# Optimization experiments

Measured on AMD Instinct MI355X. Metric: run time of the kernel, lower is better.

The kernel has to match this reference:

```python
import jax, jax.numpy as jnp
import numpy as np
from jax import lax

NB, NS, C, H, W = 16, 8, 3, 128, 128
FVDIM, K = 512, 10


def setup_inputs() -> dict:
    key = jax.random.key(0)
    ks = jax.random.split(key, 5)
    x = jax.random.normal(ks[0], (NB, NS, C, H, W), dtype=jnp.float32)
    nslice = jax.random.randint(ks[1], (NB,), 1, NS + 1, dtype=jnp.int64)  # at least 1 valid slice
    conv_w = jax.random.normal(ks[2], (FVDIM, C, 7, 7), dtype=jnp.float32) * 0.05
    conv_b = jnp.zeros((FVDIM,), dtype=jnp.float32)
    q0 = jnp.ones((1, FVDIM), dtype=jnp.float32)  # L1Aggregator init: ones
    proj_w = jax.random.normal(ks[3], (K, FVDIM), dtype=jnp.float32) * 0.02
    proj_b = jnp.zeros((K,), dtype=jnp.float32)
    return {"x": x, "nslice": nslice, "conv_w": conv_w, "conv_b": conv_b,
            "q0": q0, "proj_w": proj_w, "proj_b": proj_b}


def _extract(x, conv_w, conv_b):
    # stand-in for extractor.Resnet(4): conv(7x7, stride 4) -> ReLU -> global avg pool
    nb, ns = x.shape[:2]
    xf = x.reshape(nb * ns, C, H, W)
    y = lax.conv_general_dilated(xf, conv_w, (4, 4), 'SAME',
                                 dimension_numbers=('NCHW', 'OIHW', 'NCHW'))
    y = jax.nn.relu(y + conv_b[None, :, None, None])
    fvs = jnp.mean(y, axis=(2, 3))          # (nb*ns, fvdim)
    return fvs.reshape(nb, ns, FVDIM)


def reference(x, nslice, conv_w, conv_b, q0, proj_w, proj_b):
    # x: (nb, ns, c, h, w); ragged over ns via nslice -> masked batched attention
    fvs = _extract(x, conv_w, conv_b)                       # (nb, ns, d)
    mask = jnp.arange(NS)[None, :] < nslice[:, None]        # (nb, ns)
    scores = jnp.einsum('d,bsd->bs', q0[0], fvs)            # ek = q0 @ fvs^T per sample
    scores = jnp.where(mask, scores, -jnp.inf)
    ak = jax.nn.softmax(scores, axis=1)                     # per-sample softmax over valid slices
    r0 = jnp.einsum('bs,bsd->bd', ak, fvs)                  # (nb, d)
    return jax.nn.sigmoid(r0 @ proj_w.T + proj_b)           # (nb, k)
```

## Files before the change

### kernel.cpp

```cpp
#include <hip/hip_runtime.h>

#define NB 16
#define NS 8
#define NIMG (NB*NS)
#define CIN 3
#define HWDIM 128
#define FV 512
#define KOUT 10
#define STRIPS 4
#define WIN_ROWS (CIN*35)
#define WIN_STRIDE 136
#define NKT 6
#define WTB_ELEMS (NKT*32*64*8)

typedef __attribute__((ext_vector_type(8))) short bf16x8;
typedef __attribute__((ext_vector_type(4))) float f32x4;

__device__ __forceinline__ unsigned short f2bf(float f) {
    unsigned int u = __float_as_uint(f);
    u = (u + 0x7FFFu + ((u >> 16) & 1u)) >> 16;
    return (unsigned short)u;
}

__global__ void wprep_kernel(const float* __restrict__ cw,
                             unsigned short* __restrict__ wtb) {
    int i = blockIdx.x * 256 + threadIdx.x;
    int j  = i & 7;
    int l  = (i >> 3) & 63;
    int nt = (i >> 9) & 31;
    int kt = i >> 14;
    int oc = nt * 16 + (l & 15);
    int kb = kt * 4 + (l >> 4);
    unsigned short v = 0;
    if (kb < 21 && j < 7) {
        int ic = kb / 7, ky = kb - 7 * ic;
        v = f2bf(cw[(size_t)oc * 147 + ic * 49 + ky * 7 + j]);
    }
    wtb[i] = v;
}

__global__ __launch_bounds__(256, 2) void conv_mfma_kernel(
    const float* __restrict__ x, const unsigned short* __restrict__ wtb,
    const float* __restrict__ cb, float* __restrict__ partial)
{
    __shared__ unsigned short win[WIN_ROWS * WIN_STRIDE];

    int wg = blockIdx.x, img = wg >> 2, strip = wg & 3, tid = threadIdx.x;
    const float* ximg = x + (size_t)img * (CIN * HWDIM * HWDIM);
    int gr0 = strip * 32 - 1;

    for (int i = tid; i < WIN_ROWS * WIN_STRIDE; i += 256) {
        int row = i / WIN_STRIDE, s = i - row * WIN_STRIDE;
        int ic = row / 35, rr = row - ic * 35;
        int c = s - 1, gr = gr0 + rr;
        float v = 0.f;
        if ((unsigned)c < (unsigned)HWDIM && (unsigned)gr < (unsigned)HWDIM)
            v = ximg[(ic * HWDIM + gr) * HWDIM + c];
        win[i] = f2bf(v);
    }
    __syncthreads();

    int l = tid & 63, wv = tid >> 6;
    int m15 = l & 15, kgrp = l >> 4;

    int rowbase[NKT];
#pragma unroll
    for (int kt = 0; kt < NKT; ++kt) {
        int kb = kt * 4 + kgrp;
        int ic = (kb < 21) ? kb / 7 : 0;
        int ky = (kb < 21) ? kb - 7 * ic : 0;
        rowbase[kt] = ic * 35 + ky;
    }

    for (int ncol = 0; ncol < 2; ++ncol) {
        int nbase = (wv * 2 + ncol) * 64;

        bf16x8 bf[NKT][4];
#pragma unroll
        for (int kt = 0; kt < NKT; ++kt)
#pragma unroll
            for (int nt = 0; nt < 4; ++nt) {
                int ntile = (nbase >> 4) + nt;
                bf[kt][nt] = *(const bf16x8*)(wtb +
                    (((size_t)(kt * 32 + ntile) * 64 + l) << 3));
            }
        float bias[4];
#pragma unroll
        for (int nt = 0; nt < 4; ++nt) bias[nt] = cb[nbase + nt * 16 + m15];
        float pool[4] = {0.f, 0.f, 0.f, 0.f};

        for (int mst = 0; mst < 4; ++mst) {
            f32x4 acc[4][4];
            const f32x4 z = {0.f, 0.f, 0.f, 0.f};
#pragma unroll
            for (int mt = 0; mt < 4; ++mt)
#pragma unroll
                for (int nt = 0; nt < 4; ++nt) acc[mt][nt] = z;

#pragma unroll
            for (int kt = 0; kt < NKT; ++kt) {
                bf16x8 at[4];
#pragma unroll
                for (int mt = 0; mt < 4; ++mt) {
                    int row = rowbase[kt] + (mst * 2 + (mt >> 1)) * 4;
                    const unsigned short* p = win + row * WIN_STRIDE + 8 * m15 + 4 * (mt & 1);
                    union { unsigned long long q[2]; bf16x8 v; } u;
                    u.q[0] = *(const unsigned long long*)(p);
                    u.q[1] = *(const unsigned long long*)(p + 4);
                    at[mt] = u.v;
                }
#pragma unroll
                for (int mt = 0; mt < 4; ++mt)
#pragma unroll
                    for (int nt = 0; nt < 4; ++nt)
                        acc[mt][nt] = __builtin_amdgcn_mfma_f32_16x16x32_bf16(
                            at[mt], bf[kt][nt], acc[mt][nt], 0, 0, 0);
            }
#pragma unroll
            for (int mt = 0; mt < 4; ++mt)
#pragma unroll
                for (int nt = 0; nt < 4; ++nt)
#pragma unroll
                    for (int r = 0; r < 4; ++r)
                        pool[nt] += fmaxf(acc[mt][nt][r] + bias[nt], 0.f);
        }
#pragma unroll
        for (int nt = 0; nt < 4; ++nt) {
            float v = pool[nt];
            v += __shfl_xor(v, 16);
            v += __shfl_xor(v, 32);
            if (l < 16) partial[(size_t)wg * FV + nbase + nt * 16 + m15] = v;
        }
    }
}

__global__ __launch_bounds__(256) void head_kernel(
    const float* __restrict__ partial, const int* __restrict__ nslice,
    const float* __restrict__ q0, const float* __restrict__ pw,
    const float* __restrict__ pb, float* __restrict__ out)
{
    __shared__ float fvs[NS][FV];
    __shared__ float sc[NS];
    __shared__ float r0[FV];
    __shared__ float red2[4];
    int b = blockIdx.x;
    int tid = threadIdx.x;

    for (int i = tid; i < NS * FV; i += 256) {
        int s = i >> 9, d = i & 511;
        const float* pp = partial + (size_t)((b * NS + s) * STRIPS) * FV + d;
        float v = pp[0] + pp[FV] + pp[2 * FV] + pp[3 * FV];
        fvs[s][d] = v * (1.f / 1024.f);
    }
    __syncthreads();

    int grp = tid >> 5, l32 = tid & 31;
    float sdot = 0.f;
    for (int d = l32; d < FV; d += 32) sdot += q0[d] * fvs[grp][d];
    sdot += __shfl_down(sdot, 16, 32);
    sdot += __shfl_down(sdot, 8, 32);
    sdot += __shfl_down(sdot, 4, 32);
    sdot += __shfl_down(sdot, 2, 32);
    sdot += __shfl_down(sdot, 1, 32);
    if (l32 == 0) sc[grp] = sdot;
    __syncthreads();

    int ns = nslice[b];
    float m = -3.0e38f;
    for (int s = 0; s < NS; ++s) if (s < ns) m = fmaxf(m, sc[s]);
    float ak[NS]; float se = 0.f;
    for (int s = 0; s < NS; ++s) {
        float e = (s < ns) ? expf(sc[s] - m) : 0.f;
        ak[s] = e; se += e;
    }
    float inv = 1.f / se;

    for (int d = tid; d < FV; d += 256) {
        float v = 0.f;
        for (int s = 0; s < NS; ++s) v += ak[s] * fvs[s][d];
        r0[d] = v * inv;
    }
    __syncthreads();

    int wid = tid >> 6, lane = tid & 63;
    for (int k = 0; k < KOUT; ++k) {
        float p = 0.f;
        for (int d = tid; d < FV; d += 256) p += r0[d] * pw[k * FV + d];
        p += __shfl_down(p, 32);
        p += __shfl_down(p, 16);
        p += __shfl_down(p, 8);
        p += __shfl_down(p, 4);
        p += __shfl_down(p, 2);
        p += __shfl_down(p, 1);
        if (lane == 0) red2[wid] = p;
        __syncthreads();
        if (tid == 0) {
            float t = red2[0] + red2[1] + red2[2] + red2[3] + pb[k];
            out[b * KOUT + k] = 1.f / (1.f + expf(-t));
        }
        __syncthreads();
    }
}

extern "C" void kernel_launch(void* const* d_in, const int* in_sizes, int n_in,
                              void* d_out, int out_size, void* d_ws, size_t ws_size,
                              hipStream_t stream) {
    (void)in_sizes; (void)n_in; (void)out_size; (void)ws_size;
    const float* x      = (const float*)d_in[0];
    const int*   nslice = (const int*)d_in[1];
    const float* cw     = (const float*)d_in[2];
    const float* cb     = (const float*)d_in[3];
    const float* q0     = (const float*)d_in[4];
    const float* pw     = (const float*)d_in[5];
    const float* pb     = (const float*)d_in[6];
    float* out = (float*)d_out;

    float* partial = (float*)d_ws;
    unsigned short* wtb = (unsigned short*)(partial + (size_t)NIMG * STRIPS * FV);

    wprep_kernel<<<WTB_ELEMS / 256, 256, 0, stream>>>(cw, wtb);
    conv_mfma_kernel<<<NIMG * STRIPS, 256, 0, stream>>>(x, wtb, cb, partial);
    head_kernel<<<NB, 256, 0, stream>>>(partial, nslice, q0, pw, pb, out);
}
```

Before: 136.2 us.

## Split conv into eight row strips, vectorize window load, simplify head reduction

Each image is now split into eight 16-output-row strips instead of four, which doubles the workgroup count to 1024. Shared memory per block shrinks, and launch bounds rise to four blocks per CU to improve occupancy and load balance. The input window is loaded with float4 reads and the padding columns are zeroed separately. The head kernel sums strip partials with float4 loads and gives each wavefront its own output so the per-k block barriers go away. The cost is more halo rows loaded per output and twice as many partial sums to write and reduce.

```diff
diff --git a/kernel.cpp b/kernel.cpp
--- a/kernel.cpp
+++ b/kernel.cpp
@@ -7,8 +7,10 @@
 #define HWDIM 128
 #define FV 512
 #define KOUT 10
-#define STRIPS 4
-#define WIN_ROWS (CIN*35)
+#define STRIPS 8
+#define SROWS 4
+#define WROWS 19
+#define WIN_ROWS (CIN*WROWS)
 #define WIN_STRIDE 136
 #define NKT 6
 #define WTB_ELEMS (NKT*32*64*8)
@@ -39,24 +41,33 @@
     wtb[i] = v;
 }
 
-__global__ __launch_bounds__(256, 2) void conv_mfma_kernel(
+__global__ __launch_bounds__(256, 4) void conv_mfma_kernel(
     const float* __restrict__ x, const unsigned short* __restrict__ wtb,
     const float* __restrict__ cb, float* __restrict__ partial)
 {
     __shared__ unsigned short win[WIN_ROWS * WIN_STRIDE];
 
-    int wg = blockIdx.x, img = wg >> 2, strip = wg & 3, tid = threadIdx.x;
+    int wg = blockIdx.x, img = wg >> 3, strip = wg & 7, tid = threadIdx.x;
     const float* ximg = x + (size_t)img * (CIN * HWDIM * HWDIM);
-    int gr0 = strip * 32 - 1;
-
-    for (int i = tid; i < WIN_ROWS * WIN_STRIDE; i += 256) {
-        int row = i / WIN_STRIDE, s = i - row * WIN_STRIDE;
-        int ic = row / 35, rr = row - ic * 35;
-        int c = s - 1, gr = gr0 + rr;
-        float v = 0.f;
-        if ((unsigned)c < (unsigned)HWDIM && (unsigned)gr < (unsigned)HWDIM)
-            v = ximg[(ic * HWDIM + gr) * HWDIM + c];
-        win[i] = f2bf(v);
+    int gr0 = strip * 16 - 1;
+
+    for (int i = tid; i < WIN_ROWS * 8; i += 256) {
+        int row = i >> 3, z = i & 7;
+        int slot = z ? 128 + z : 0;
+        win[row * WIN_STRIDE + slot] = 0;
+    }
+    for (int i = tid; i < WIN_ROWS * 32; i += 256) {
+        int row = i >> 5, e = i & 31;
+        int ic = row / WROWS, rr = row - ic * WROWS;
+        int gr = gr0 + rr;
+        float4 v = {0.f, 0.f, 0.f, 0.f};
+        if ((unsigned)gr < (unsigned)HWDIM)
+            v = *(const float4*)(ximg + ((size_t)(ic * HWDIM + gr) << 7) + 4 * e);
+        int base = row * WIN_STRIDE + 1 + 4 * e;
+        win[base + 0] = f2bf(v.x);
+        win[base + 1] = f2bf(v.y);
+        win[base + 2] = f2bf(v.z);
+        win[base + 3] = f2bf(v.w);
     }
     __syncthreads();
 
@@ -69,7 +80,7 @@
         int kb = kt * 4 + kgrp;
         int ic = (kb < 21) ? kb / 7 : 0;
         int ky = (kb < 21) ? kb - 7 * ic : 0;
-        rowbase[kt] = ic * 35 + ky;
+        rowbase[kt] = ic * WROWS + ky;
     }
 
     for (int ncol = 0; ncol < 2; ++ncol) {
@@ -89,7 +100,7 @@
         for (int nt = 0; nt < 4; ++nt) bias[nt] = cb[nbase + nt * 16 + m15];
         float pool[4] = {0.f, 0.f, 0.f, 0.f};
 
-        for (int mst = 0; mst < 4; ++mst) {
+        for (int mst = 0; mst < 2; ++mst) {
             f32x4 acc[4][4];
             const f32x4 z = {0.f, 0.f, 0.f, 0.f};
 #pragma unroll
@@ -142,15 +153,21 @@
     __shared__ float fvs[NS][FV];
     __shared__ float sc[NS];
     __shared__ float r0[FV];
-    __shared__ float red2[4];
     int b = blockIdx.x;
     int tid = threadIdx.x;
 
-    for (int i = tid; i < NS * FV; i += 256) {
-        int s = i >> 9, d = i & 511;
-        const float* pp = partial + (size_t)((b * NS + s) * STRIPS) * FV + d;
-        float v = pp[0] + pp[FV] + pp[2 * FV] + pp[3 * FV];
-        fvs[s][d] = v * (1.f / 1024.f);
+    for (int i = tid; i < NS * (FV / 4); i += 256) {
+        int s = i >> 7, d4 = i & 127;
+        const float* pp = partial + ((size_t)(b * NS + s) * STRIPS) * FV + 4 * d4;
+        float4 a = {0.f, 0.f, 0.f, 0.f};
+#pragma unroll
+        for (int st = 0; st < STRIPS; ++st) {
+            float4 v = *(const float4*)(pp + (size_t)st * FV);
+            a.x += v.x; a.y += v.y; a.z += v.z; a.w += v.w;
+        }
+        const float sc4 = 1.f / 1024.f;
+        float4 r = {a.x * sc4, a.y * sc4, a.z * sc4, a.w * sc4};
+        *(float4*)&fvs[s][4 * d4] = r;
     }
     __syncthreads();
 
@@ -182,23 +199,18 @@
     }
     __syncthreads();
 
-    int wid = tid >> 6, lane = tid & 63;
-    for (int k = 0; k < KOUT; ++k) {
+    int wv = tid >> 6, l = tid & 63;
+    for (int k = wv; k < KOUT; k += 4) {
         float p = 0.f;
-        for (int d = tid; d < FV; d += 256) p += r0[d] * pw[k * FV + d];
+#pragma unroll
+        for (int t = 0; t < 8; ++t) p += r0[l + 64 * t] * pw[k * FV + l + 64 * t];
         p += __shfl_down(p, 32);
         p += __shfl_down(p, 16);
         p += __shfl_down(p, 8);
         p += __shfl_down(p, 4);
         p += __shfl_down(p, 2);
         p += __shfl_down(p, 1);
-        if (lane == 0) red2[wid] = p;
-        __syncthreads();
-        if (tid == 0) {
-            float t = red2[0] + red2[1] + red2[2] + red2[3] + pb[k];
-            out[b * KOUT + k] = 1.f / (1.f + expf(-t));
-        }
-        __syncthreads();
+        if (l == 0) out[b * KOUT + k] = 1.f / (1.f + expf(-(p + pb[k])));
     }
 }
 
```

Result: slower. 459.6 us (+237.4%).
